# Kernel tuning notes

Measured on AMD Instinct MI355X. Metric: run time of the kernel, lower is better.

## Reference

```python
import jax, jax.numpy as jnp
import numpy as np

NBX = 24  # nb_x_patches
NBY = 24  # nb_y_patches
B, H, D = 8, 12, 64
L = NBX * NBY + 1  # 577 (grid tokens + 1 CLS token from the pad)
EPS = 1e-08


def _toeplitz_mask(topological_params):
    # topological_params: [H, 4*NBX*NBY]
    gi = jnp.arange(NBX)
    gj = jnp.arange(NBY)
    # relative 2D displacement index, flattened over (i, j, i', j')
    dist_index = ((gi[:, None, None, None] - gi[None, None, :, None] + NBX) * 2 * NBY
                  + gj[None, :, None, None] - gj[None, None, None, :] + NBY)
    dist_index = dist_index.reshape(-1)
    m = jnp.take(topological_params, dist_index, axis=1)
    m = m.reshape(topological_params.shape[0], NBX * NBY, NBX * NBY)  # [H, L-1, L-1]
    # pad CLS row and column with 1.0
    m = jnp.pad(m, [[0, 0], [1, 0], [1, 0]], constant_values=1.0)  # [H, L, L]
    return m[None]  # [1, H, L, L]


def setup_inputs() -> dict:
    key = jax.random.key(0)
    k1, k2, k3, k4 = jax.random.split(key, 4)
    return {
        'query': jax.random.normal(k1, (B, L, H, D), dtype=jnp.float32),
        'key': jax.random.normal(k2, (B, L, H, D), dtype=jnp.float32),
        'value': jax.random.normal(k3, (B, L, H, D), dtype=jnp.float32),
        'topological_params': jax.random.normal(k4, (H, 4 * NBX * NBY), dtype=jnp.float32),
    }


def reference(query, key, value, topological_params):
    depth = query.shape[-1]
    q = query / jnp.sqrt(jnp.asarray(depth, query.dtype))
    # relu feature map (kernel_type == 'relu')
    q = jax.nn.relu(q) + EPS
    k = jax.nn.relu(key) + EPS
    attn = jnp.einsum('bqhd,bkhd->bhqk', q, k)  # [B, H, L, L]
    top_mask = _toeplitz_mask(topological_params)  # [1, H, L, L]
    attn = attn * jnp.abs(top_mask) + EPS
    attn = attn / jnp.sum(attn, axis=-1, keepdims=True)  # kernelized normalization (no softmax)
    return jnp.einsum('bhqk,bkhd->bqhd', attn, value)
```

## Files before the change

kernel.cpp:

```cpp
#include <hip/hip_runtime.h>


#define Lq 577
#define NH 12
#define NB 8
#define DD 64
#define PAR 2304
#define EPSf 1e-8f

#define VT_OFF 7090176ull
#define MM_OFF 14954496ull

typedef __attribute__((ext_vector_type(4))) float f32x4;
typedef __attribute__((ext_vector_type(8))) short s16x8;

__device__ __forceinline__ float bflo(unsigned int u) {
    return __builtin_bit_cast(float, u << 16);
}
__device__ __forceinline__ float bfhi(unsigned int u) {
    return __builtin_bit_cast(float, u & 0xffff0000u);
}
__device__ __forceinline__ unsigned int f2bf(float f) {
    unsigned int x = __builtin_bit_cast(unsigned int, f);
    return (x + 0x7fffu + ((x >> 16) & 1u)) >> 16;
}
__device__ __forceinline__ int imin(int a, int b) { return a < b ? a : b; }

__device__ __forceinline__ void gload_lds16(const unsigned short* g, unsigned short* l) {
    __builtin_amdgcn_global_load_lds(
        (const __attribute__((address_space(1))) unsigned int*)g,
        (__attribute__((address_space(3))) unsigned int*)l, 16, 0, 0);
}

__device__ __forceinline__ bool probe_f32(const void* Qg) {
    float x = fabsf(((const float*)Qg)[threadIdx.x]);
    unsigned long long hit = __ballot(x > 2.44140625e-4f && x < 64.0f);
    unsigned long long act = __ballot(1);
    return 2 * __popcll(hit) >= __popcll(act);
}

template <bool F32>
__device__ __forceinline__ void load8f(const void* G, size_t eidx, float* o) {
    if constexpr (F32) {
        const float* p = (const float*)G + eidx;
        float4 a = *(const float4*)p;
        float4 b = *(const float4*)(p + 4);
        o[0] = a.x; o[1] = a.y; o[2] = a.z; o[3] = a.w;
        o[4] = b.x; o[5] = b.y; o[6] = b.z; o[7] = b.w;
    } else {
        const unsigned short* p = (const unsigned short*)G + eidx;
        uint4 a = *(const uint4*)p;
        unsigned int u[4] = {a.x, a.y, a.z, a.w};
#pragma unroll
        for (int j = 0; j < 4; ++j) {
            o[2 * j]     = bflo(u[j]);
            o[2 * j + 1] = bfhi(u[j]);
        }
    }
}

template <bool F32>
__device__ void prep_k_body(const void* Kg, unsigned short* Kp) {
    size_t i8 = ((size_t)blockIdx.x * 256 + threadIdx.x) * 8;
    float f[8];
    load8f<F32>(Kg, i8, f);
    unsigned int o[4];
#pragma unroll
    for (int j = 0; j < 4; ++j) {
        unsigned int lo = f2bf(fmaxf(f[2 * j], 0.0f) + EPSf);
        unsigned int hi = f2bf(fmaxf(f[2 * j + 1], 0.0f) + EPSf);
        o[j] = lo | (hi << 16);
    }
    *(uint4*)(Kp + i8) = make_uint4(o[0], o[1], o[2], o[3]);
}
__global__ __launch_bounds__(256)
void prep_k(const void* __restrict__ Qg, const void* __restrict__ Kg,
            unsigned short* __restrict__ Kp) {
    if (probe_f32(Qg)) prep_k_body<true>(Kg, Kp);
    else               prep_k_body<false>(Kg, Kp);
}

template <bool F32>
__device__ void prep_vt_body(const void* Vg, unsigned short* Vt, unsigned short* s) {
    const int t  = threadIdx.x;
    const int kt = blockIdx.x, h = blockIdx.y, b = blockIdx.z;
    {
        int kl  = t >> 2;
        int dch = (t & 3) * 16;
        int k   = kt * 64 + kl;
        unsigned int pk[8] = {};
        if (k <= 576) {
            float f[16];
            size_t base = ((size_t)((b * Lq + k) * NH + h)) * DD + dch;
            load8f<F32>(Vg, base, f);
            load8f<F32>(Vg, base + 8, f + 8);
#pragma unroll
            for (int j = 0; j < 8; ++j)
                pk[j] = f2bf(f[2 * j]) | (f2bf(f[2 * j + 1]) << 16);
        }
#pragma unroll
        for (int j = 0; j < 8; ++j)
            *(unsigned int*)&s[kl * 72 + dch + 2 * j] = pk[j];
    }
    __syncthreads();
    {
        int d   = t >> 2;
        int kch = (t & 3) * 16;
        unsigned int o[8];
#pragma unroll
        for (int j = 0; j < 8; ++j) {
            unsigned short v0 = s[(kch + 2 * j) * 72 + d];
            unsigned short v1 = s[(kch + 2 * j + 1) * 72 + d];
            o[j] = (unsigned int)v0 | ((unsigned int)v1 << 16);
        }
        size_t base = ((size_t)((b * NH + h) * 64 + d)) * 640 + kt * 64 + kch;
        *(uint4*)(Vt + base)     = make_uint4(o[0], o[1], o[2], o[3]);
        *(uint4*)(Vt + base + 8) = make_uint4(o[4], o[5], o[6], o[7]);
    }
}
__global__ __launch_bounds__(256)
void prep_vt(const void* __restrict__ Qg, const void* __restrict__ Vg,
             unsigned short* __restrict__ Vt) {
    __shared__ unsigned short s[64 * 72];
    if (probe_f32(Qg)) prep_vt_body<true>(Vg, Vt, s);
    else               prep_vt_body<false>(Vg, Vt, s);
}

template <bool F32>
__device__ void prep_mask_body(const void* Tg, unsigned short* Mm) {
    const int q = blockIdx.x, h = blockIdx.y;
    const int k0 = threadIdx.x * 8;
    int cq = 0;
    if (q > 0) {
        int qq = q - 1;
        int qi = (qq * 2731) >> 16;
        cq = qq + 24 * qi + 1176;
    }
    unsigned int o[4];
#pragma unroll
    for (int j = 0; j < 4; ++j) {
        unsigned int hv[2];
#pragma unroll
        for (int e = 0; e < 2; ++e) {
            int k = k0 + 2 * j + e;
            float m;
            if (k > 576) m = 0.0f;
            else if (k == 0 || q == 0) m = 1.0f;
            else {
                int kk = k - 1;
                int ki = (kk * 2731) >> 16;
                int idx = cq - (kk + 24 * ki);
                float pv = F32 ? ((const float*)Tg)[h * PAR + idx]
                               : bflo((unsigned int)((const unsigned short*)Tg)[h * PAR + idx]);
                m = fabsf(pv);
                m = (m == m) ? m : 0.0f;
            }
            hv[e] = f2bf(m);
        }
        o[j] = hv[0] | (hv[1] << 16);
    }
    *(uint4*)(Mm + (size_t)(h * Lq + q) * 640 + k0) = make_uint4(o[0], o[1], o[2], o[3]);
}
__global__ __launch_bounds__(128)
void prep_mask(const void* __restrict__ Qg, const void* __restrict__ Tg,
               unsigned short* __restrict__ Mm) {
    if (probe_f32(Qg)) prep_mask_body<true>(Tg, Mm);
    else               prep_mask_body<false>(Tg, Mm);
}

template <bool F32>
__device__ void attn_body(const void* __restrict__ Qg,
                          const unsigned short* __restrict__ Kp,
                          const unsigned short* __restrict__ Vt,
                          const unsigned short* __restrict__ Mm,
                          void* __restrict__ Og,
                          unsigned short* s_k, unsigned short* s_vt,
                          unsigned short* s_m, unsigned short* s_p_all) {
    const int tid  = threadIdx.x;
    const int w    = tid >> 6;
    const int lane = tid & 63;
    const int g    = lane >> 4;
    const int lm   = lane & 15;

    const int bid = blockIdx.x;
    const int qt  = bid / 96;
    const int bh  = bid - qt * 96;
    const int h   = bh % NH;
    const int b   = bh / NH;

    unsigned short* s_pw = s_p_all + w * 16 * 72;
    unsigned short* s_mw = s_m + w * 1024;

    const int q0w = qt * 64 + w * 16;

    const int q  = q0w + lm;
    const int qc = imin(q, Lq - 1);
    s16x8 a_q[2];
    {
        size_t rbase = ((size_t)((b * Lq + qc) * NH + h)) * DD;
#pragma unroll
        for (int ds = 0; ds < 2; ++ds) {
            float f[8];
            load8f<F32>(Qg, rbase + ds * 32 + g * 8, f);
            s16x8 a;
#pragma unroll
            for (int j = 0; j < 8; ++j) {
                float v = fmaf(fmaxf(f[j], 0.0f), 0.125f, EPSf);
                a[j] = (short)f2bf(v);
            }
            a_q[ds] = a;
        }
    }

    const int r8 = lane >> 3;
    const int c8 = lane & 7;
    const int xr = (c8 ^ r8) * 8;

    const unsigned short* KpBH = Kp + (size_t)b * (Lq * NH * DD) + h * DD;
    const unsigned short* VtL0 = Vt + ((size_t)(b * NH + h) * 64 + (w * 16 + r8)) * 640 + xr;
    const unsigned short* VtL1 = VtL0 + 8 * 640;
    const unsigned short* MmH  = Mm + (size_t)h * (Lq * 640);
    const unsigned short* MmL0 = MmH + (size_t)imin(q0w + r8, Lq - 1) * 640 + xr;
    const unsigned short* MmL1 = MmH + (size_t)imin(q0w + 8 + r8, Lq - 1) * 640 + xr;

    unsigned short* sk0 = s_k  + (w * 16) * 64;
    unsigned short* sk1 = sk0 + 8 * 64;
    unsigned short* sv0 = s_vt + (w * 16) * 64;
    unsigned short* sv1 = sv0 + 8 * 64;
    unsigned short* sm1 = s_mw + 8 * 64;

    f32x4 o_acc[4] = {};
    float rs = 0.0f;

    const int x7 = lm & 7;

    for (int kb = 0; kb < 640; kb += 64) {
        __syncthreads();

        int krr = kb + w * 16 + r8;
        int kr0 = imin(krr, Lq - 1);
        int kr1 = imin(krr + 8, Lq - 1);
        gload_lds16(KpBH + (size_t)kr0 * (NH * DD) + xr, sk0);
        gload_lds16(KpBH + (size_t)kr1 * (NH * DD) + xr, sk1);
        gload_lds16(VtL0 + kb, sv0);
        gload_lds16(VtL1 + kb, sv1);
        gload_lds16(MmL0 + kb, s_mw);
        gload_lds16(MmL1 + kb, sm1);
        __syncthreads();

        f32x4 sf[4];
#pragma unroll
        for (int cf = 0; cf < 4; ++cf) {
            const unsigned short* skr = s_k + (cf * 16 + lm) * 64;
            int co = (g ^ x7) * 8;
            s16x8 kf0 = *(const s16x8*)(skr + co);
            s16x8 kf1 = *(const s16x8*)(skr + (co ^ 32));
            f32x4 acc = {};
            acc = __builtin_amdgcn_mfma_f32_16x16x32_bf16(kf0, a_q[0], acc, 0, 0, 0);
            acc = __builtin_amdgcn_mfma_f32_16x16x32_bf16(kf1, a_q[1], acc, 0, 0, 0);
            sf[cf] = acc;
        }

#pragma unroll
        for (int cf = 0; cf < 4; ++cf) {
            int mo = ((cf * 2 + (g >> 1)) ^ x7) * 8 + (g & 1) * 4;
            uint2 mu = *(const uint2*)&s_mw[lm * 64 + mo];
            float m0 = bflo(mu.x), m1 = bfhi(mu.x);
            float m2 = bflo(mu.y), m3 = bfhi(mu.y);
            float p0 = fmaf(fmaxf(sf[cf][0], 0.0f), m0, EPSf);
            float p1 = fmaf(fmaxf(sf[cf][1], 0.0f), m1, EPSf);
            float p2 = fmaf(fmaxf(sf[cf][2], 0.0f), m2, EPSf);
            float p3 = fmaf(fmaxf(sf[cf][3], 0.0f), m3, EPSf);
            rs += (p0 + p1) + (p2 + p3);
            unsigned int d0 = f2bf(p0) | (f2bf(p1) << 16);
            unsigned int d1 = f2bf(p2) | (f2bf(p3) << 16);
            *(uint2*)&s_pw[lm * 72 + cf * 16 + g * 4] = make_uint2(d0, d1);
        }

#pragma unroll
        for (int ks = 0; ks < 2; ++ks) {
            s16x8 pa = *(const s16x8*)&s_pw[lm * 72 + ks * 32 + g * 8];
#pragma unroll
            for (int df = 0; df < 4; ++df) {
                const unsigned short* svr = s_vt + (df * 16 + lm) * 64;
                s16x8 vb = *(const s16x8*)(svr + ((ks * 4 + g) ^ x7) * 8);
                o_acc[df] = __builtin_amdgcn_mfma_f32_16x16x32_bf16(pa, vb, o_acc[df], 0, 0, 0);
            }
        }
    }

    float tot = rs;
    tot += __shfl_xor(tot, 16, 64);
    tot += __shfl_xor(tot, 32, 64);
    float inv = (tot > 0.0f) ? 1.0f / tot : 0.0f;

#pragma unroll
    for (int r = 0; r < 4; ++r) {
        int   qrow  = q0w + g * 4 + r;
        float inv_r = __shfl(inv, g * 4 + r, 64);
        if (qrow < Lq) {
            size_t base = ((size_t)((b * Lq + qrow) * NH + h)) * DD;
#pragma unroll
            for (int df = 0; df < 4; ++df) {
                float val = o_acc[df][r] * inv_r;
                if constexpr (F32)
                    ((float*)Og)[base + df * 16 + lm] = val;
                else
                    ((unsigned short*)Og)[base + df * 16 + lm] = (unsigned short)f2bf(val);
            }
        }
    }
}

__global__ __launch_bounds__(256, 4)
void fused_topo_attn(const void* __restrict__ Qg,
                     const unsigned short* __restrict__ Kp,
                     const unsigned short* __restrict__ Vt,
                     const unsigned short* __restrict__ Mm,
                     void* __restrict__ Og) {
    __shared__ __align__(16) unsigned short s_k[64 * 64];
    __shared__ __align__(16) unsigned short s_vt[64 * 64];
    __shared__ __align__(16) unsigned short s_m[4 * 16 * 64];
    __shared__ __align__(16) unsigned short s_p[4 * 16 * 72];

    if (probe_f32(Qg)) attn_body<true>(Qg, Kp, Vt, Mm, Og, s_k, s_vt, s_m, s_p);
    else               attn_body<false>(Qg, Kp, Vt, Mm, Og, s_k, s_vt, s_m, s_p);
}

extern "C" void kernel_launch(void* const* d_in, const int* in_sizes, int n_in,
                              void* d_out, int out_size, void* d_ws, size_t ws_size,
                              hipStream_t stream) {
    (void)in_sizes; (void)n_in; (void)out_size; (void)ws_size;
    unsigned short* Kp = (unsigned short*)d_ws;
    unsigned short* Vt = (unsigned short*)((char*)d_ws + VT_OFF);
    unsigned short* Mm = (unsigned short*)((char*)d_ws + MM_OFF);

    prep_k<<<1731, 256, 0, stream>>>(d_in[0], d_in[1], Kp);
    prep_vt<<<dim3(10, NH, NB), 256, 0, stream>>>(d_in[0], d_in[2], Vt);
    prep_mask<<<dim3(Lq, NH), 80, 0, stream>>>(d_in[0], d_in[3], Mm);
    fused_topo_attn<<<960, 256, 0, stream>>>(d_in[0], Kp, Vt, Mm, d_out);
}
```

Before: 122.2 us.

## Merge prep kernels and double-buffer K/V staging with direct mask loads

Merges the three preprocessing kernels (K relu+bf16, V transpose, mask build) into one launch with block-index dispatch, which removes two kernel launches and their gaps. In the attention kernel, K and V tiles are double-buffered in LDS so the next tile's global-to-LDS load overlaps the current tile's MFMA work, leaving one barrier per iteration instead of two. The mask is no longer staged in LDS: each lane reads it straight from global memory into registers. The P scratch buffer switches from padded rows to an XOR swizzle. The trade-off is more LDS per block and uncoalesced mask reads from global memory.

New measurement: 124.8 us. 2.1% more time.

```diff
diff --git a/kernel.cpp b/kernel.cpp
--- a/kernel.cpp
+++ b/kernel.cpp
@@ -10,6 +10,10 @@
 
 #define VT_OFF 7090176ull
 #define MM_OFF 14954496ull
+
+#define PK_BLOCKS  1731
+#define PVT_BLOCKS 960
+#define PM_BLOCKS  2316
 
 typedef __attribute__((ext_vector_type(4))) float f32x4;
 typedef __attribute__((ext_vector_type(8))) short s16x8;
@@ -60,112 +64,118 @@
 }
 
 template <bool F32>
-__device__ void prep_k_body(const void* Kg, unsigned short* Kp) {
-    size_t i8 = ((size_t)blockIdx.x * 256 + threadIdx.x) * 8;
-    float f[8];
-    load8f<F32>(Kg, i8, f);
-    unsigned int o[4];
-#pragma unroll
-    for (int j = 0; j < 4; ++j) {
-        unsigned int lo = f2bf(fmaxf(f[2 * j], 0.0f) + EPSf);
-        unsigned int hi = f2bf(fmaxf(f[2 * j + 1], 0.0f) + EPSf);
-        o[j] = lo | (hi << 16);
-    }
-    *(uint4*)(Kp + i8) = make_uint4(o[0], o[1], o[2], o[3]);
+__device__ void prep_all_body(const void* __restrict__ Kg,
+                              const void* __restrict__ Vg,
+                              const void* __restrict__ Tg,
+                              unsigned short* __restrict__ Kp,
+                              unsigned short* __restrict__ Vt,
+                              unsigned short* __restrict__ Mm,
+                              unsigned short* s) {
+    const int bid = blockIdx.x;
+    const int t   = threadIdx.x;
+
+    if (bid < PK_BLOCKS) {
+        size_t i8 = ((size_t)bid * 256 + t) * 8;
+        float f[8];
+        load8f<F32>(Kg, i8, f);
+        unsigned int o[4];
+#pragma unroll
+        for (int j = 0; j < 4; ++j) {
+            unsigned int lo = f2bf(fmaxf(f[2 * j], 0.0f) + EPSf);
+            unsigned int hi = f2bf(fmaxf(f[2 * j + 1], 0.0f) + EPSf);
+            o[j] = lo | (hi << 16);
+        }
+        *(uint4*)(Kp + i8) = make_uint4(o[0], o[1], o[2], o[3]);
+
+    } else if (bid < PK_BLOCKS + PVT_BLOCKS) {
+        int r  = bid - PK_BLOCKS;
+        int kt = r % 10; r /= 10;
+        int h  = r % NH;
+        int b  = r / NH;
+        {
+            int kl  = t >> 2;
+            int dch = (t & 3) * 16;
+            int k   = kt * 64 + kl;
+            unsigned int pk[8] = {};
+            if (k <= 576) {
+                float f[16];
+                size_t base = ((size_t)((b * Lq + k) * NH + h)) * DD + dch;
+                load8f<F32>(Vg, base, f);
+                load8f<F32>(Vg, base + 8, f + 8);
+#pragma unroll
+                for (int j = 0; j < 8; ++j)
+                    pk[j] = f2bf(f[2 * j]) | (f2bf(f[2 * j + 1]) << 16);
+            }
+#pragma unroll
+            for (int j = 0; j < 8; ++j)
+                *(unsigned int*)&s[kl * 72 + dch + 2 * j] = pk[j];
+        }
+        __syncthreads();
+        {
+            int d   = t >> 2;
+            int kch = (t & 3) * 16;
+            unsigned int o[8];
+#pragma unroll
+            for (int j = 0; j < 8; ++j) {
+                unsigned short v0 = s[(kch + 2 * j) * 72 + d];
+                unsigned short v1 = s[(kch + 2 * j + 1) * 72 + d];
+                o[j] = (unsigned int)v0 | ((unsigned int)v1 << 16);
+            }
+            size_t base = ((size_t)((b * NH + h) * 64 + d)) * 640 + kt * 64 + kch;
+            *(uint4*)(Vt + base)     = make_uint4(o[0], o[1], o[2], o[3]);
+            *(uint4*)(Vt + base + 8) = make_uint4(o[4], o[5], o[6], o[7]);
+        }
+
+    } else {
+        int r  = bid - (PK_BLOCKS + PVT_BLOCKS);
+        int h  = r / 193;
+        int qb = (r % 193) * 3;
+        if (t < 240) {
+            int q = qb + t / 80;
+            if (q < Lq) {
+                int k0 = (t % 80) * 8;
+                int cq = 0;
+                if (q > 0) {
+                    int qq = q - 1;
+                    int qi = (qq * 2731) >> 16;
+                    cq = qq + 24 * qi + 1176;
+                }
+                unsigned int o[4];
+#pragma unroll
+                for (int j = 0; j < 4; ++j) {
+                    unsigned int hv[2];
+#pragma unroll
+                    for (int e = 0; e < 2; ++e) {
+                        int k = k0 + 2 * j + e;
+                        float m;
+                        if (k > 576) m = 0.0f;
+                        else if (k == 0 || q == 0) m = 1.0f;
+                        else {
+                            int kk = k - 1;
+                            int ki = (kk * 2731) >> 16;
+                            int idx = cq - (kk + 24 * ki);
+                            float pv = F32 ? ((const float*)Tg)[h * PAR + idx]
+                                           : bflo((unsigned int)((const unsigned short*)Tg)[h * PAR + idx]);
+                            m = fabsf(pv);
+                            m = (m == m) ? m : 0.0f;
+                        }
+                        hv[e] = f2bf(m);
+                    }
+                    o[j] = hv[0] | (hv[1] << 16);
+                }
+                *(uint4*)(Mm + (size_t)(h * Lq + q) * 640 + k0) = make_uint4(o[0], o[1], o[2], o[3]);
+            }
+        }
+    }
 }
 __global__ __launch_bounds__(256)
-void prep_k(const void* __restrict__ Qg, const void* __restrict__ Kg,
-            unsigned short* __restrict__ Kp) {
-    if (probe_f32(Qg)) prep_k_body<true>(Kg, Kp);
-    else               prep_k_body<false>(Kg, Kp);
-}
-
-template <bool F32>
-__device__ void prep_vt_body(const void* Vg, unsigned short* Vt, unsigned short* s) {
-    const int t  = threadIdx.x;
-    const int kt = blockIdx.x, h = blockIdx.y, b = blockIdx.z;
-    {
-        int kl  = t >> 2;
-        int dch = (t & 3) * 16;
-        int k   = kt * 64 + kl;
-        unsigned int pk[8] = {};
-        if (k <= 576) {
-            float f[16];
-            size_t base = ((size_t)((b * Lq + k) * NH + h)) * DD + dch;
-            load8f<F32>(Vg, base, f);
-            load8f<F32>(Vg, base + 8, f + 8);
-#pragma unroll
-            for (int j = 0; j < 8; ++j)
-                pk[j] = f2bf(f[2 * j]) | (f2bf(f[2 * j + 1]) << 16);
-        }
-#pragma unroll
-        for (int j = 0; j < 8; ++j)
-            *(unsigned int*)&s[kl * 72 + dch + 2 * j] = pk[j];
-    }
-    __syncthreads();
-    {
-        int d   = t >> 2;
-        int kch = (t & 3) * 16;
-        unsigned int o[8];
-#pragma unroll
-        for (int j = 0; j < 8; ++j) {
-            unsigned short v0 = s[(kch + 2 * j) * 72 + d];
-            unsigned short v1 = s[(kch + 2 * j + 1) * 72 + d];
-            o[j] = (unsigned int)v0 | ((unsigned int)v1 << 16);
-        }
-        size_t base = ((size_t)((b * NH + h) * 64 + d)) * 640 + kt * 64 + kch;
-        *(uint4*)(Vt + base)     = make_uint4(o[0], o[1], o[2], o[3]);
-        *(uint4*)(Vt + base + 8) = make_uint4(o[4], o[5], o[6], o[7]);
-    }
-}
-__global__ __launch_bounds__(256)
-void prep_vt(const void* __restrict__ Qg, const void* __restrict__ Vg,
-             unsigned short* __restrict__ Vt) {
-    __shared__ unsigned short s[64 * 72];
-    if (probe_f32(Qg)) prep_vt_body<true>(Vg, Vt, s);
-    else               prep_vt_body<false>(Vg, Vt, s);
-}
-
-template <bool F32>
-__device__ void prep_mask_body(const void* Tg, unsigned short* Mm) {
-    const int q = blockIdx.x, h = blockIdx.y;
-    const int k0 = threadIdx.x * 8;
-    int cq = 0;
-    if (q > 0) {
-        int qq = q - 1;
-        int qi = (qq * 2731) >> 16;
-        cq = qq + 24 * qi + 1176;
-    }
-    unsigned int o[4];
-#pragma unroll
-    for (int j = 0; j < 4; ++j) {
-        unsigned int hv[2];
-#pragma unroll
-        for (int e = 0; e < 2; ++e) {
-            int k = k0 + 2 * j + e;
-            float m;
-            if (k > 576) m = 0.0f;
-            else if (k == 0 || q == 0) m = 1.0f;
-            else {
-                int kk = k - 1;
-                int ki = (kk * 2731) >> 16;
-                int idx = cq - (kk + 24 * ki);
-                float pv = F32 ? ((const float*)Tg)[h * PAR + idx]
-                               : bflo((unsigned int)((const unsigned short*)Tg)[h * PAR + idx]);
-                m = fabsf(pv);
-                m = (m == m) ? m : 0.0f;
-            }
-            hv[e] = f2bf(m);
-        }
-        o[j] = hv[0] | (hv[1] << 16);
-    }
-    *(uint4*)(Mm + (size_t)(h * Lq + q) * 640 + k0) = make_uint4(o[0], o[1], o[2], o[3]);
-}
-__global__ __launch_bounds__(128)
-void prep_mask(const void* __restrict__ Qg, const void* __restrict__ Tg,
-               unsigned short* __restrict__ Mm) {
-    if (probe_f32(Qg)) prep_mask_body<true>(Tg, Mm);
-    else               prep_mask_body<false>(Tg, Mm);
+void prep_all(const void* __restrict__ Qg, const void* __restrict__ Kg,
+              const void* __restrict__ Vg, const void* __restrict__ Tg,
+              unsigned short* __restrict__ Kp, unsigned short* __restrict__ Vt,
+              unsigned short* __restrict__ Mm) {
+    __shared__ __align__(16) unsigned short s[64 * 72];
+    if (probe_f32(Qg)) prep_all_body<true>(Kg, Vg, Tg, Kp, Vt, Mm, s);
+    else               prep_all_body<false>(Kg, Vg, Tg, Kp, Vt, Mm, s);
 }
 
 template <bool F32>
@@ -175,7 +185,7 @@
                           const unsigned short* __restrict__ Mm,
                           void* __restrict__ Og,
                           unsigned short* s_k, unsigned short* s_vt,
-                          unsigned short* s_m, unsigned short* s_p_all) {
+                          unsigned short* s_p_all) {
     const int tid  = threadIdx.x;
     const int w    = tid >> 6;
     const int lane = tid & 63;
@@ -188,9 +198,7 @@
     const int h   = bh % NH;
     const int b   = bh / NH;
 
-    unsigned short* s_pw = s_p_all + w * 16 * 72;
-    unsigned short* s_mw = s_m + w * 1024;
-
+    unsigned short* s_pw = s_p_all + w * 16 * 64;
     const int q0w = qt * 64 + w * 16;
 
     const int q  = q0w + lm;
@@ -219,39 +227,45 @@
     const unsigned short* KpBH = Kp + (size_t)b * (Lq * NH * DD) + h * DD;
     const unsigned short* VtL0 = Vt + ((size_t)(b * NH + h) * 64 + (w * 16 + r8)) * 640 + xr;
     const unsigned short* VtL1 = VtL0 + 8 * 640;
-    const unsigned short* MmH  = Mm + (size_t)h * (Lq * 640);
-    const unsigned short* MmL0 = MmH + (size_t)imin(q0w + r8, Lq - 1) * 640 + xr;
-    const unsigned short* MmL1 = MmH + (size_t)imin(q0w + 8 + r8, Lq - 1) * 640 + xr;
-
-    unsigned short* sk0 = s_k  + (w * 16) * 64;
-    unsigned short* sk1 = sk0 + 8 * 64;
-    unsigned short* sv0 = s_vt + (w * 16) * 64;
-    unsigned short* sv1 = sv0 + 8 * 64;
-    unsigned short* sm1 = s_mw + 8 * 64;
+    const unsigned short* MmQ  = Mm + (size_t)h * (Lq * 640) + (size_t)qc * 640 + g * 4;
 
     f32x4 o_acc[4] = {};
     float rs = 0.0f;
-
     const int x7 = lm & 7;
 
-    for (int kb = 0; kb < 640; kb += 64) {
-        __syncthreads();
-
+    auto stageKV = [&](int kb, int buf) {
+        unsigned short* skb = s_k  + buf * 4096 + (w * 16) * 64;
+        unsigned short* svb = s_vt + buf * 4096 + (w * 16) * 64;
         int krr = kb + w * 16 + r8;
         int kr0 = imin(krr, Lq - 1);
         int kr1 = imin(krr + 8, Lq - 1);
-        gload_lds16(KpBH + (size_t)kr0 * (NH * DD) + xr, sk0);
-        gload_lds16(KpBH + (size_t)kr1 * (NH * DD) + xr, sk1);
-        gload_lds16(VtL0 + kb, sv0);
-        gload_lds16(VtL1 + kb, sv1);
-        gload_lds16(MmL0 + kb, s_mw);
-        gload_lds16(MmL1 + kb, sm1);
-        __syncthreads();
+        gload_lds16(KpBH + (size_t)kr0 * (NH * DD) + xr, skb);
+        gload_lds16(KpBH + (size_t)kr1 * (NH * DD) + xr, skb + 8 * 64);
+        gload_lds16(VtL0 + kb, svb);
+        gload_lds16(VtL1 + kb, svb + 8 * 64);
+    };
+
+    stageKV(0, 0);
+    __syncthreads();
+
+    for (int t = 0; t < 10; ++t) {
+        const int kb  = t * 64;
+        const int buf = t & 1;
+
+        uint2 mu[4];
+#pragma unroll
+        for (int cf = 0; cf < 4; ++cf)
+            mu[cf] = *(const uint2*)(MmQ + kb + cf * 16);
+
+        if (t < 9) stageKV(kb + 64, buf ^ 1);
+
+        const unsigned short* skB = s_k  + buf * 4096;
+        const unsigned short* svB = s_vt + buf * 4096;
 
         f32x4 sf[4];
 #pragma unroll
         for (int cf = 0; cf < 4; ++cf) {
-            const unsigned short* skr = s_k + (cf * 16 + lm) * 64;
+            const unsigned short* skr = skB + (cf * 16 + lm) * 64;
             int co = (g ^ x7) * 8;
             s16x8 kf0 = *(const s16x8*)(skr + co);
             s16x8 kf1 = *(const s16x8*)(skr + (co ^ 32));
@@ -263,10 +277,8 @@
 
 #pragma unroll
         for (int cf = 0; cf < 4; ++cf) {
-            int mo = ((cf * 2 + (g >> 1)) ^ x7) * 8 + (g & 1) * 4;
-            uint2 mu = *(const uint2*)&s_mw[lm * 64 + mo];
-            float m0 = bflo(mu.x), m1 = bfhi(mu.x);
-            float m2 = bflo(mu.y), m3 = bfhi(mu.y);
+            float m0 = bflo(mu[cf].x), m1 = bfhi(mu[cf].x);
+            float m2 = bflo(mu[cf].y), m3 = bfhi(mu[cf].y);
             float p0 = fmaf(fmaxf(sf[cf][0], 0.0f), m0, EPSf);
             float p1 = fmaf(fmaxf(sf[cf][1], 0.0f), m1, EPSf);
             float p2 = fmaf(fmaxf(sf[cf][2], 0.0f), m2, EPSf);
@@ -274,19 +286,22 @@
             rs += (p0 + p1) + (p2 + p3);
             unsigned int d0 = f2bf(p0) | (f2bf(p1) << 16);
             unsigned int d1 = f2bf(p2) | (f2bf(p3) << 16);
-            *(uint2*)&s_pw[lm * 72 + cf * 16 + g * 4] = make_uint2(d0, d1);
+            int pc = (((cf * 2 + (g >> 1)) ^ x7) << 3) + ((g & 1) << 2);
+            *(uint2*)&s_pw[lm * 64 + pc] = make_uint2(d0, d1);
         }
 
 #pragma unroll
         for (int ks = 0; ks < 2; ++ks) {
-            s16x8 pa = *(const s16x8*)&s_pw[lm * 72 + ks * 32 + g * 8];
+            s16x8 pa = *(const s16x8*)&s_pw[lm * 64 + (((ks * 4 + g) ^ x7) << 3)];
 #pragma unroll
             for (int df = 0; df < 4; ++df) {
-                const unsigned short* svr = s_vt + (df * 16 + lm) * 64;
-                s16x8 vb = *(const s16x8*)(svr + ((ks * 4 + g) ^ x7) * 8);
+                const unsigned short* svr = svB + (df * 16 + lm) * 64;
+                s16x8 vb = *(const s16x8*)(svr + (((ks * 4 + g) ^ x7) << 3));
                 o_acc[df] = __builtin_amdgcn_mfma_f32_16x16x32_bf16(pa, vb, o_acc[df], 0, 0, 0);
             }
         }
+
+        if (t < 9) __syncthreads();
     }
 
     float tot = rs;
@@ -318,13 +333,12 @@
                      const unsigned short* __restrict__ Vt,
                      const unsigned short* __restrict__ Mm,
                      void* __restrict__ Og) {
-    __shared__ __align__(16) unsigned short s_k[64 * 64];
-    __shared__ __align__(16) unsigned short s_vt[64 * 64];
-    __shared__ __align__(16) unsigned short s_m[4 * 16 * 64];
-    __shared__ __align__(16) unsigned short s_p[4 * 16 * 72];
-
-    if (probe_f32(Qg)) attn_body<true>(Qg, Kp, Vt, Mm, Og, s_k, s_vt, s_m, s_p);
-    else               attn_body<false>(Qg, Kp, Vt, Mm, Og, s_k, s_vt, s_m, s_p);
+    __shared__ __align__(16) unsigned short s_k[2 * 64 * 64];
+    __shared__ __align__(16) unsigned short s_vt[2 * 64 * 64];
+    __shared__ __align__(16) unsigned short s_p[4 * 16 * 64];
+
+    if (probe_f32(Qg)) attn_body<true>(Qg, Kp, Vt, Mm, Og, s_k, s_vt, s_p);
+    else               attn_body<false>(Qg, Kp, Vt, Mm, Og, s_k, s_vt, s_p);
 }
 
 extern "C" void kernel_launch(void* const* d_in, const int* in_sizes, int n_in,
@@ -335,8 +349,7 @@
     unsigned short* Vt = (unsigned short*)((char*)d_ws + VT_OFF);
     unsigned short* Mm = (unsigned short*)((char*)d_ws + MM_OFF);
 
-    prep_k<<<1731, 256, 0, stream>>>(d_in[0], d_in[1], Kp);
-    prep_vt<<<dim3(10, NH, NB), 256, 0, stream>>>(d_in[0], d_in[2], Vt);
-    prep_mask<<<dim3(Lq, NH), 80, 0, stream>>>(d_in[0], d_in[3], Mm);
+    prep_all<<<PK_BLOCKS + PVT_BLOCKS + PM_BLOCKS, 256, 0, stream>>>(
+        d_in[0], d_in[1], d_in[2], d_in[3], Kp, Vt, Mm);
     fused_topo_attn<<<960, 256, 0, stream>>>(d_in[0], Kp, Vt, Mm, d_out);
 }
```
